# Optimization experiments

Measured on AMD Instinct MI355X. Metric: run time of the kernel, lower is better.

Reference implementation:

```python
import jax, jax.numpy as jnp
import numpy as np

NUM_WORDS = 35000
EMBED_DIM = 100
MAX_LEN = 80
BATCH = 2048
UNITS = 512


def setup_inputs() -> dict:
    key = jax.random.key(0)
    ks = jax.random.split(key, 7)
    inputs = jax.random.randint(ks[0], (BATCH, MAX_LEN), 0, NUM_WORDS)
    emb_table = jax.random.normal(ks[1], (NUM_WORDS, EMBED_DIM), jnp.float32) * 0.05
    W_xh = jax.random.normal(ks[2], (EMBED_DIM, UNITS), jnp.float32) * (1.0 / np.sqrt(EMBED_DIM))
    W_hh = jax.random.normal(ks[3], (UNITS, UNITS), jnp.float32) * (1.0 / np.sqrt(UNITS))
    b_h = jnp.zeros((UNITS,), jnp.float32)
    W_out = jax.random.normal(ks[4], (UNITS, 1), jnp.float32) * (1.0 / np.sqrt(UNITS))
    b_out = jnp.zeros((1,), jnp.float32)
    return {"inputs": inputs, "emb_table": emb_table, "W_xh": W_xh,
            "W_hh": W_hh, "b_h": b_h, "W_out": W_out, "b_out": b_out}


def reference(inputs, emb_table, W_xh, W_hh, b_h, W_out, b_out):
    # Embedding lookup: [B, T, D]
    x = emb_table[inputs]
    # Precompute input projection for all timesteps (batched GEMM): [B, T, U]
    xw = jnp.einsum('btd,du->btu', x, W_xh) + b_h
    h0 = jnp.zeros((inputs.shape[0], W_hh.shape[0]), x.dtype)

    def step(h, xt):
        # SimpleRNNCell (inference, dropout off): h' = tanh(x@W_xh + b + h@W_hh)
        h_new = jnp.tanh(xt + h @ W_hh)
        return h_new, None

    # scan over time axis; carry only the [B, U] hidden state
    h_last, _ = jax.lax.scan(step, h0, jnp.swapaxes(xw, 0, 1))
    logits = h_last @ W_out + b_out  # [B, 1]
    return jax.nn.sigmoid(logits)
```

## Files before the change

kernel.cpp:

```cpp
#include <hip/hip_runtime.h>
#include <hip/hip_bf16.h>


#define T_LEN   80
#define EMB_D   100
#define UNITS   512
#define ROWS    16
#define NBLK    128
#define NTHR    512
#define NT      4
#define KSH     16
#define KSX     4
#define RKS     6

typedef __bf16 bf16x8 __attribute__((ext_vector_type(8)));
typedef float  f32x4  __attribute__((ext_vector_type(4)));

__device__ __forceinline__ float fast_tanh(float x) {
    float e = __builtin_amdgcn_exp2f(x * 2.8853900817779268f);
    return 1.0f - 2.0f * __builtin_amdgcn_rcpf(1.0f + e);
}

__global__ void prep_kernel(const float* __restrict__ Whh,
                            const float* __restrict__ Wxh,
                            __bf16* __restrict__ Wt, __bf16* __restrict__ Xt) {
    __shared__ float tile[32][33];
    const int tx = threadIdx.x & 31, ty = threadIdx.x >> 5;
    const int b = blockIdx.x;
    if (b < 256) {
        const int k0 = (b & 15) * 32, n0 = (b >> 4) * 32;
        #pragma unroll
        for (int i = 0; i < 4; ++i)
            tile[ty + 8 * i][tx] = Whh[(k0 + ty + 8 * i) * UNITS + n0 + tx];
        __syncthreads();
        #pragma unroll
        for (int i = 0; i < 4; ++i) {
            const int n = ty + 8 * i;
            Wt[(n0 + n) * UNITS + k0 + tx] = (__bf16)tile[tx][n];
        }
    } else {
        const int bb = b - 256;
        const int k0 = (bb & 3) * 32, n0 = (bb >> 2) * 32;
        #pragma unroll
        for (int i = 0; i < 4; ++i) {
            const int k = k0 + ty + 8 * i;
            tile[ty + 8 * i][tx] = (k < EMB_D) ? Wxh[k * UNITS + n0 + tx] : 0.0f;
        }
        __syncthreads();
        #pragma unroll
        for (int i = 0; i < 4; ++i) {
            const int n = ty + 8 * i;
            Xt[(n0 + n) * 128 + k0 + tx] = (__bf16)tile[tx][n];
        }
    }
}

__global__ __launch_bounds__(NTHR, 1)
void rnn_kernel(const int*   __restrict__ inputs,
                const float* __restrict__ emb,
                const float* __restrict__ bh,
                const float* __restrict__ Wout,
                const float* __restrict__ bout,
                const __bf16* __restrict__ Wt,
                const __bf16* __restrict__ Xt,
                float*       __restrict__ out)
{
    __shared__ alignas(16) __bf16 hbuf[2][16 * UNITS];
    __shared__ alignas(16) __bf16 xbuf[2][16 * 128];

    const int tid  = threadIdx.x;
    const int wave = tid >> 6;
    const int lane = tid & 63;
    const int q    = lane >> 4;
    const int ln   = lane & 15;
    const int e7   = ln & 7;
    const int qa   = q ^ (e7 & 3);
    const int kx   = e7 >> 2;
    const int q8   = q << 3;
    const int r0   = blockIdx.x * ROWS;

    int coff[NT], cxff[NT];
    float bhv[NT];
    #pragma unroll
    for (int nt = 0; nt < NT; ++nt) {
        const int c = (wave << 6) + (nt << 4) + ln;
        coff[nt] = c * UNITS;
        cxff[nt] = c * 128;
        bhv[nt]  = bh[c];
    }

    bf16x8 whh[RKS][NT];
    bf16x8 wxh[KSX][NT];
    #pragma unroll
    for (int nt = 0; nt < NT; ++nt) {
        #pragma unroll
        for (int ks = 0; ks < RKS; ++ks)
            whh[ks][nt] = *(const bf16x8*)(Wt + coff[nt] + (ks << 5) + q8);
        #pragma unroll
        for (int ks = 0; ks < KSX; ++ks)
            wxh[ks][nt] = *(const bf16x8*)(Xt + cxff[nt] + (ks << 5) + q8);
    }

    {
        int4 z; z.x = z.y = z.z = z.w = 0;
        int4* hp = (int4*)&hbuf[0][0];
        #pragma unroll
        for (int i = 0; i < 4; ++i) hp[tid + i * NTHR] = z;
        int4* xp = (int4*)&xbuf[0][0];
        xp[tid] = z;
    }
    __syncthreads();

    auto stage = [&](int t, __bf16* xb) {
        #pragma unroll
        for (int rr = 0; rr < 2; ++rr) {
            const int r = wave + (rr << 3);
            const int idxv = inputs[(r0 + r) * T_LEN + t];
            const float* er = emb + (size_t)idxv * EMB_D;
            const int k0 = lane;
            xb[(r << 7) + ((((k0 >> 3) ^ (r & 7)) << 3) | (k0 & 7))] = (__bf16)er[k0];
            const int k1 = lane + 64;
            if (k1 < EMB_D)
                xb[(r << 7) + ((((k1 >> 3) ^ (r & 7)) << 3) | (k1 & 7))] = (__bf16)er[k1];
        }
    };

    auto step = [&](const __bf16* hb_r, const __bf16* xb_r, __bf16* hb_w) {
        bf16x8 sB[2][NT];
        #pragma unroll
        for (int nt = 0; nt < NT; ++nt)
            sB[0][nt] = *(const bf16x8*)(Wt + coff[nt] + (RKS << 5) + q8);
        #pragma unroll
        for (int nt = 0; nt < NT; ++nt)
            sB[1][nt] = *(const bf16x8*)(Wt + coff[nt] + ((RKS + 1) << 5) + q8);

        f32x4 acc[NT];
        #pragma unroll
        for (int nt = 0; nt < NT; ++nt) {
            f32x4 a = {bhv[nt], bhv[nt], bhv[nt], bhv[nt]};
            acc[nt] = a;
        }

        const int xbase = (ln << 7) + (qa << 3);
        #pragma unroll
        for (int ks = 0; ks < KSX; ++ks) {
            bf16x8 a = *(const bf16x8*)&xb_r[xbase + ((ks ^ kx) << 5)];
            #pragma unroll
            for (int nt = 0; nt < NT; ++nt)
                acc[nt] = __builtin_amdgcn_mfma_f32_16x16x32_bf16(a, wxh[ks][nt], acc[nt], 0, 0, 0);
        }
        const int hbase = (ln << 9) + (qa << 3);
        #pragma unroll
        for (int ks = 0; ks < RKS; ++ks) {
            bf16x8 a = *(const bf16x8*)&hb_r[hbase + ((ks ^ kx) << 5)];
            #pragma unroll
            for (int nt = 0; nt < NT; ++nt)
                acc[nt] = __builtin_amdgcn_mfma_f32_16x16x32_bf16(a, whh[ks][nt], acc[nt], 0, 0, 0);
        }
        #pragma unroll
        for (int ks = RKS; ks < KSH; ++ks) {
            const int s = (ks - RKS) & 1;
            bf16x8 a = *(const bf16x8*)&hb_r[hbase + ((ks ^ kx) << 5)];
            #pragma unroll
            for (int nt = 0; nt < NT; ++nt)
                acc[nt] = __builtin_amdgcn_mfma_f32_16x16x32_bf16(a, sB[s][nt], acc[nt], 0, 0, 0);
            if (ks + 2 < KSH) {
                #pragma unroll
                for (int nt = 0; nt < NT; ++nt)
                    sB[s][nt] = *(const bf16x8*)(Wt + coff[nt] + ((ks + 2) << 5) + q8);
            }
        }
        #pragma unroll
        for (int nt = 0; nt < NT; ++nt) {
            const int cc = (wave << 3) + (nt << 1) + (ln >> 3);
            #pragma unroll
            for (int i = 0; i < 4; ++i) {
                const int row = (q << 2) + i;
                hb_w[(row << 9) + (((cc ^ (row & 7)) << 3) | (ln & 7))] =
                    (__bf16)fast_tanh(acc[nt][i]);
            }
        }
    };

    stage(0, xbuf[0]);
    __syncthreads();

    #pragma unroll 1
    for (int t = 0; t < T_LEN; t += 2) {
        stage(t + 1, xbuf[1]);
        step(hbuf[0], xbuf[0], hbuf[1]);
        __syncthreads();
        if (t + 2 < T_LEN) stage(t + 2, xbuf[0]);
        step(hbuf[1], xbuf[1], hbuf[0]);
        __syncthreads();
    }

    #pragma unroll
    for (int rr = 0; rr < 2; ++rr) {
        const int m = wave + (rr << 3);
        const bf16x8 hv = *(const bf16x8*)&hbuf[0][(m << 9) + ((lane ^ wave) << 3)];
        float s = 0.0f;
        #pragma unroll
        for (int j = 0; j < 8; ++j)
            s += (float)hv[j] * Wout[(lane << 3) + j];
        #pragma unroll
        for (int off = 32; off > 0; off >>= 1)
            s += __shfl_down(s, off, 64);
        if (lane == 0) {
            const float logit = s + bout[0];
            out[r0 + m] = __builtin_amdgcn_rcpf(
                1.0f + __builtin_amdgcn_exp2f(-logit * 1.4426950408889634f));
        }
    }
}

extern "C" void kernel_launch(void* const* d_in, const int* in_sizes, int n_in,
                              void* d_out, int out_size, void* d_ws, size_t ws_size,
                              hipStream_t stream) {
    __bf16* Wt = (__bf16*)d_ws;
    __bf16* Xt = Wt + UNITS * UNITS;
    prep_kernel<<<dim3(320), dim3(256), 0, stream>>>(
        (const float*)d_in[3],
        (const float*)d_in[2],
        Wt, Xt);
    rnn_kernel<<<dim3(NBLK), dim3(NTHR), 0, stream>>>(
        (const int*)d_in[0],
        (const float*)d_in[1],
        (const float*)d_in[4],
        (const float*)d_in[5],
        (const float*)d_in[6],
        Wt, Xt,
        (float*)d_out);
}
```

Baseline: 1.107 ms.

## Process 32 rows per block with 4 waves covering 128 columns each

Blocks now handle 32 batch rows with 4 waves of 256 threads over 64 blocks. Each wave computes two 16-row M tiles across 8 N tiles, so every W_hh/W_xh fragment loaded from registers or global memory is reused twice. The streamed-weight prefetch depth grows to 3 and fewer W_hh slices stay resident in registers. This halves the number of blocks, leaving many CUs idle, and raises register pressure from doubled accumulators, which may limit latency hiding.

```diff
diff --git a/kernel.cpp b/kernel.cpp
--- a/kernel.cpp
+++ b/kernel.cpp
@@ -5,13 +5,15 @@
 #define T_LEN   80
 #define EMB_D   100
 #define UNITS   512
-#define ROWS    16
-#define NBLK    128
-#define NTHR    512
-#define NT      4
+#define ROWS    32
+#define NBLK    64
+#define NTHR    256
+#define NW      4
+#define NT      8
 #define KSH     16
 #define KSX     4
-#define RKS     6
+#define RKS     4
+#define SDEPTH  3
 
 typedef __bf16 bf16x8 __attribute__((ext_vector_type(8)));
 typedef float  f32x4  __attribute__((ext_vector_type(4)));
@@ -65,8 +67,8 @@
                 const __bf16* __restrict__ Xt,
                 float*       __restrict__ out)
 {
-    __shared__ alignas(16) __bf16 hbuf[2][16 * UNITS];
-    __shared__ alignas(16) __bf16 xbuf[2][16 * 128];
+    __shared__ alignas(16) __bf16 hbuf[2][ROWS * UNITS];
+    __shared__ alignas(16) __bf16 xbuf[2][ROWS * 128];
 
     const int tid  = threadIdx.x;
     const int wave = tid >> 6;
@@ -79,42 +81,43 @@
     const int q8   = q << 3;
     const int r0   = blockIdx.x * ROWS;
 
-    int coff[NT], cxff[NT];
+    int   woff[NT];
     float bhv[NT];
     #pragma unroll
     for (int nt = 0; nt < NT; ++nt) {
-        const int c = (wave << 6) + (nt << 4) + ln;
-        coff[nt] = c * UNITS;
-        cxff[nt] = c * 128;
-        bhv[nt]  = bh[c];
+        const int col = (wave << 7) + (nt << 4) + ln;
+        woff[nt] = col * UNITS + q8;
+        bhv[nt]  = bh[col];
     }
 
     bf16x8 whh[RKS][NT];
     bf16x8 wxh[KSX][NT];
     #pragma unroll
     for (int nt = 0; nt < NT; ++nt) {
+        const int xo = ((wave << 7) + (nt << 4) + ln) * 128 + q8;
         #pragma unroll
         for (int ks = 0; ks < RKS; ++ks)
-            whh[ks][nt] = *(const bf16x8*)(Wt + coff[nt] + (ks << 5) + q8);
+            whh[ks][nt] = *(const bf16x8*)(Wt + woff[nt] + (ks << 5));
         #pragma unroll
         for (int ks = 0; ks < KSX; ++ks)
-            wxh[ks][nt] = *(const bf16x8*)(Xt + cxff[nt] + (ks << 5) + q8);
+            wxh[ks][nt] = *(const bf16x8*)(Xt + xo + (ks << 5));
     }
 
     {
         int4 z; z.x = z.y = z.z = z.w = 0;
         int4* hp = (int4*)&hbuf[0][0];
         #pragma unroll
-        for (int i = 0; i < 4; ++i) hp[tid + i * NTHR] = z;
+        for (int i = 0; i < 8; ++i) hp[tid + i * NTHR] = z;
         int4* xp = (int4*)&xbuf[0][0];
-        xp[tid] = z;
+        #pragma unroll
+        for (int i = 0; i < 4; ++i) xp[tid + i * NTHR] = z;
     }
     __syncthreads();
 
     auto stage = [&](int t, __bf16* xb) {
         #pragma unroll
-        for (int rr = 0; rr < 2; ++rr) {
-            const int r = wave + (rr << 3);
+        for (int rr = 0; rr < 8; ++rr) {
+            const int r = (wave << 3) + rr;
             const int idxv = inputs[(r0 + r) * T_LEN + t];
             const float* er = emb + (size_t)idxv * EMB_D;
             const int k0 = lane;
@@ -126,60 +129,75 @@
     };
 
     auto step = [&](const __bf16* hb_r, const __bf16* xb_r, __bf16* hb_w) {
-        bf16x8 sB[2][NT];
-        #pragma unroll
-        for (int nt = 0; nt < NT; ++nt)
-            sB[0][nt] = *(const bf16x8*)(Wt + coff[nt] + (RKS << 5) + q8);
-        #pragma unroll
-        for (int nt = 0; nt < NT; ++nt)
-            sB[1][nt] = *(const bf16x8*)(Wt + coff[nt] + ((RKS + 1) << 5) + q8);
-
-        f32x4 acc[NT];
-        #pragma unroll
-        for (int nt = 0; nt < NT; ++nt) {
-            f32x4 a = {bhv[nt], bhv[nt], bhv[nt], bhv[nt]};
-            acc[nt] = a;
-        }
-
-        const int xbase = (ln << 7) + (qa << 3);
+        bf16x8 sB[SDEPTH][NT];
+        #pragma unroll
+        for (int p = 0; p < SDEPTH; ++p)
+            #pragma unroll
+            for (int nt = 0; nt < NT; ++nt)
+                sB[p][nt] = *(const bf16x8*)(Wt + woff[nt] + ((RKS + p) << 5));
+
+        f32x4 acc[2][NT];
+        #pragma unroll
+        for (int mt = 0; mt < 2; ++mt)
+            #pragma unroll
+            for (int nt = 0; nt < NT; ++nt) {
+                f32x4 a = {bhv[nt], bhv[nt], bhv[nt], bhv[nt]};
+                acc[mt][nt] = a;
+            }
+
+        const int xb0 = (ln << 7) + (qa << 3);
         #pragma unroll
         for (int ks = 0; ks < KSX; ++ks) {
-            bf16x8 a = *(const bf16x8*)&xb_r[xbase + ((ks ^ kx) << 5)];
-            #pragma unroll
-            for (int nt = 0; nt < NT; ++nt)
-                acc[nt] = __builtin_amdgcn_mfma_f32_16x16x32_bf16(a, wxh[ks][nt], acc[nt], 0, 0, 0);
-        }
-        const int hbase = (ln << 9) + (qa << 3);
+            const bf16x8 a0 = *(const bf16x8*)&xb_r[xb0 + ((ks ^ kx) << 5)];
+            const bf16x8 a1 = *(const bf16x8*)&xb_r[xb0 + (16 << 7) + ((ks ^ kx) << 5)];
+            #pragma unroll
+            for (int nt = 0; nt < NT; ++nt)
+                acc[0][nt] = __builtin_amdgcn_mfma_f32_16x16x32_bf16(a0, wxh[ks][nt], acc[0][nt], 0, 0, 0);
+            #pragma unroll
+            for (int nt = 0; nt < NT; ++nt)
+                acc[1][nt] = __builtin_amdgcn_mfma_f32_16x16x32_bf16(a1, wxh[ks][nt], acc[1][nt], 0, 0, 0);
+        }
+        const int hb0 = (ln << 9) + (qa << 3);
         #pragma unroll
         for (int ks = 0; ks < RKS; ++ks) {
-            bf16x8 a = *(const bf16x8*)&hb_r[hbase + ((ks ^ kx) << 5)];
-            #pragma unroll
-            for (int nt = 0; nt < NT; ++nt)
-                acc[nt] = __builtin_amdgcn_mfma_f32_16x16x32_bf16(a, whh[ks][nt], acc[nt], 0, 0, 0);
+            const bf16x8 a0 = *(const bf16x8*)&hb_r[hb0 + ((ks ^ kx) << 5)];
+            const bf16x8 a1 = *(const bf16x8*)&hb_r[hb0 + (16 << 9) + ((ks ^ kx) << 5)];
+            #pragma unroll
+            for (int nt = 0; nt < NT; ++nt)
+                acc[0][nt] = __builtin_amdgcn_mfma_f32_16x16x32_bf16(a0, whh[ks][nt], acc[0][nt], 0, 0, 0);
+            #pragma unroll
+            for (int nt = 0; nt < NT; ++nt)
+                acc[1][nt] = __builtin_amdgcn_mfma_f32_16x16x32_bf16(a1, whh[ks][nt], acc[1][nt], 0, 0, 0);
         }
         #pragma unroll
         for (int ks = RKS; ks < KSH; ++ks) {
-            const int s = (ks - RKS) & 1;
-            bf16x8 a = *(const bf16x8*)&hb_r[hbase + ((ks ^ kx) << 5)];
-            #pragma unroll
-            for (int nt = 0; nt < NT; ++nt)
-                acc[nt] = __builtin_amdgcn_mfma_f32_16x16x32_bf16(a, sB[s][nt], acc[nt], 0, 0, 0);
-            if (ks + 2 < KSH) {
+            const int s = (ks - RKS) % SDEPTH;
+            const bf16x8 a0 = *(const bf16x8*)&hb_r[hb0 + ((ks ^ kx) << 5)];
+            const bf16x8 a1 = *(const bf16x8*)&hb_r[hb0 + (16 << 9) + ((ks ^ kx) << 5)];
+            #pragma unroll
+            for (int nt = 0; nt < NT; ++nt)
+                acc[0][nt] = __builtin_amdgcn_mfma_f32_16x16x32_bf16(a0, sB[s][nt], acc[0][nt], 0, 0, 0);
+            #pragma unroll
+            for (int nt = 0; nt < NT; ++nt)
+                acc[1][nt] = __builtin_amdgcn_mfma_f32_16x16x32_bf16(a1, sB[s][nt], acc[1][nt], 0, 0, 0);
+            if (ks + SDEPTH < KSH) {
                 #pragma unroll
                 for (int nt = 0; nt < NT; ++nt)
-                    sB[s][nt] = *(const bf16x8*)(Wt + coff[nt] + ((ks + 2) << 5) + q8);
+                    sB[s][nt] = *(const bf16x8*)(Wt + woff[nt] + ((ks + SDEPTH) << 5));
             }
         }
         #pragma unroll
-        for (int nt = 0; nt < NT; ++nt) {
-            const int cc = (wave << 3) + (nt << 1) + (ln >> 3);
-            #pragma unroll
-            for (int i = 0; i < 4; ++i) {
-                const int row = (q << 2) + i;
-                hb_w[(row << 9) + (((cc ^ (row & 7)) << 3) | (ln & 7))] =
-                    (__bf16)fast_tanh(acc[nt][i]);
+        for (int mt = 0; mt < 2; ++mt)
+            #pragma unroll
+            for (int nt = 0; nt < NT; ++nt) {
+                const int cc = (wave << 4) + (nt << 1) + (ln >> 3);
+                #pragma unroll
+                for (int i = 0; i < 4; ++i) {
+                    const int row = (mt << 4) + (q << 2) + i;
+                    hb_w[(row << 9) + (((cc ^ (row & 7)) << 3) | (ln & 7))] =
+                        (__bf16)fast_tanh(acc[mt][nt][i]);
+                }
             }
-        }
     };
 
     stage(0, xbuf[0]);
@@ -196,9 +214,9 @@
     }
 
     #pragma unroll
-    for (int rr = 0; rr < 2; ++rr) {
-        const int m = wave + (rr << 3);
-        const bf16x8 hv = *(const bf16x8*)&hbuf[0][(m << 9) + ((lane ^ wave) << 3)];
+    for (int rr = 0; rr < 8; ++rr) {
+        const int m = (wave << 3) + rr;
+        const bf16x8 hv = *(const bf16x8*)&hbuf[0][(m << 9) + ((lane ^ (m & 7)) << 3)];
         float s = 0.0f;
         #pragma unroll
         for (int j = 0; j < 8; ++j)
```

Result: slower. 1.838 ms (+66.0%).
